# Performance work log

Measured on AMD Instinct MI355X. Metric: run time of the kernel, lower is better.

## Reference

```python
import jax, jax.numpy as jnp
import numpy as np

EPS = 1e-6


def setup_inputs() -> dict:
    key = jax.random.key(0)
    k1, k2, k3, k4 = jax.random.split(key, 4)
    B, N, D = 8, 4096, 512
    x = jax.random.normal(k1, (B, N, D), dtype=jnp.float32)
    # torch nn.Linear(dim, 3*dim, bias=False): weight shape [3D, D], y = x @ W.T
    w_qkv = jax.random.normal(k2, (3 * D, D), dtype=jnp.float32) * (1.0 / np.sqrt(D))
    w_proj = jax.random.normal(k3, (D, D), dtype=jnp.float32) * (1.0 / np.sqrt(D))
    b_proj = jax.random.normal(k4, (D,), dtype=jnp.float32) * 0.01
    return {"x": x, "w_qkv": w_qkv, "w_proj": w_proj, "b_proj": b_proj, "heads": 8}


def reference(x, w_qkv, w_proj, b_proj, heads):
    B, N, D = x.shape
    H = heads
    d = D // H
    # qkv projection -> (3, B, H, N, d)
    qkv = (x @ w_qkv.T).reshape(B, N, 3, H, d).transpose(2, 0, 3, 1, 4)
    q, k, v = qkv[0], qkv[1], qkv[2]
    # elu+1 feature map (positive features)
    q = jax.nn.elu(q) + 1.0 + EPS
    k = jax.nn.elu(k) + 1.0 + EPS
    # kv summary: [B,H,d,d]
    kv = jnp.einsum('bhnd,bhne->bhde', k, v)
    # denominator: q . sum_n(k) -> [B,H,N]
    denom = jnp.einsum('bhnd,bhd->bhn', q, k.sum(axis=2))
    out = jnp.einsum('bhnd,bhde->bhne', q, kv) / (denom[..., None] + EPS)
    out = out.transpose(0, 2, 1, 3).reshape(B, N, D)
    return out @ w_proj.T + b_proj
```

## Files before the change

kernel.cpp:

```cpp
#include <hip/hip_runtime.h>
#include <hip/hip_bf16.h>
#include <math.h>

#define EPSF 1e-6f

constexpr int Bc = 8;
constexpr int Nc = 4096;
constexpr int Dc = 512;
constexpr int QKVC = 3 * Dc;

typedef __attribute__((ext_vector_type(8))) short short8v;
typedef __attribute__((ext_vector_type(8))) unsigned short ushort8v;
typedef __attribute__((ext_vector_type(4))) float float4v;

__device__ __forceinline__ unsigned short f2bf(float f) {
    union { float f; unsigned int u; } v; v.f = f;
    unsigned int u = v.u;
    return (unsigned short)((u + 0x7fffu + ((u >> 16) & 1u)) >> 16);
}
__device__ __forceinline__ float bf2f(unsigned short h) {
    union { unsigned int u; float f; } v; v.u = ((unsigned int)h) << 16;
    return v.f;
}

typedef __attribute__((address_space(1))) const void gvoid_t;
typedef __attribute__((address_space(3))) void lvoid_t;
__device__ __forceinline__ void llds16(const void* g, void* l) {
    __builtin_amdgcn_global_load_lds((gvoid_t*)g, (lvoid_t*)l, 16, 0, 0);
}

__global__ __launch_bounds__(256) void cvt_f32_bf16(
    const float* __restrict__ in, unsigned short* __restrict__ out, int n8)
{
    int i = blockIdx.x * 256 + threadIdx.x;
    if (i >= n8) return;
    float4 a = reinterpret_cast<const float4*>(in)[2 * i];
    float4 b = reinterpret_cast<const float4*>(in)[2 * i + 1];
    ushort8v o;
    o[0] = f2bf(a.x); o[1] = f2bf(a.y); o[2] = f2bf(a.z); o[3] = f2bf(a.w);
    o[4] = f2bf(b.x); o[5] = f2bf(b.y); o[6] = f2bf(b.z); o[7] = f2bf(b.w);
    reinterpret_cast<ushort8v*>(out)[i] = o;
}

__global__ __launch_bounds__(256) void cvt_weights(
    const float* __restrict__ wq, const float* __restrict__ wp,
    unsigned short* __restrict__ wqo, unsigned short* __restrict__ wpo)
{
    const int i = blockIdx.x * 256 + threadIdx.x;
    const int NQ = 1536 * 512 / 8;
    const float* src; unsigned short* dst; int idx;
    if (i < NQ) { src = wq; dst = wqo; idx = i; }
    else        { src = wp; dst = wpo; idx = i - NQ; }
    float4 a = reinterpret_cast<const float4*>(src)[2 * idx];
    float4 b = reinterpret_cast<const float4*>(src)[2 * idx + 1];
    ushort8v o;
    o[0] = f2bf(a.x); o[1] = f2bf(a.y); o[2] = f2bf(a.z); o[3] = f2bf(a.w);
    o[4] = f2bf(b.x); o[5] = f2bf(b.y); o[6] = f2bf(b.z); o[7] = f2bf(b.w);
    reinterpret_cast<ushort8v*>(dst)[idx] = o;
}

__global__ __launch_bounds__(512, 2) void gemm_qkv(
    const unsigned short* __restrict__ A,
    const unsigned short* __restrict__ Bm,
    unsigned short* __restrict__ Cout)
{
    constexpr int LDA = 512, LDB = 512, LDC = 1536;
    constexpr int NT = 8;
    __shared__ unsigned short ring[3][24576];

    const int t = threadIdx.x;
    const int orig = blockIdx.x;
    const int wg = (orig & 7) * 192 + (orig >> 3);
    const int bm = (wg / 12) * 256;
    const int bn = (wg % 12) * 128;

    const int w = t >> 6, lane = t & 63;
    const int ln = lane & 15, g = lane >> 4;
    const int wr = (w >> 1) * 64;
    const int wc = (w & 1) * 64;
    const int l7 = ln & 7;

    const int rs = t >> 3;
    const int ci = t & 7;
    const int swz = ci ^ (rs & 7);
    const unsigned short* As0 = A + (size_t)(bm + rs) * LDA + swz * 8;
    const unsigned short* As1 = A + (size_t)(bm + 64 + rs) * LDA + swz * 8;
    const unsigned short* As2 = A + (size_t)(bm + 128 + rs) * LDA + swz * 8;
    const unsigned short* As3 = A + (size_t)(bm + 192 + rs) * LDA + swz * 8;
    const unsigned short* Bs0 = Bm + (size_t)(bn + rs) * LDB + swz * 8;
    const unsigned short* Bs1 = Bm + (size_t)(bn + 64 + rs) * LDB + swz * 8;

#define STAGEQ(Tt) do {                                                        \
        const int k0_ = (Tt) * 64;                                             \
        unsigned short* dA_ = &ring[(Tt) % 3][0];                              \
        unsigned short* dB_ = &ring[(Tt) % 3][16384];                          \
        llds16(As0 + k0_, dA_ + (size_t)t * 8);                                \
        llds16(As1 + k0_, dA_ + (size_t)(512 + t) * 8);                        \
        llds16(As2 + k0_, dA_ + (size_t)(1024 + t) * 8);                       \
        llds16(As3 + k0_, dA_ + (size_t)(1536 + t) * 8);                       \
        llds16(Bs0 + k0_, dB_ + (size_t)t * 8);                                \
        llds16(Bs1 + k0_, dB_ + (size_t)(512 + t) * 8);                        \
    } while (0)

    float4v acc[4][4];
#pragma unroll
    for (int i = 0; i < 4; ++i)
#pragma unroll
        for (int j = 0; j < 4; ++j) acc[i][j] = {0.f, 0.f, 0.f, 0.f};

    STAGEQ(0);
    STAGEQ(1);
    asm volatile("s_waitcnt vmcnt(6)" ::: "memory");
    __builtin_amdgcn_s_barrier();
    __builtin_amdgcn_sched_barrier(0);

#pragma unroll
    for (int T = 0; T < NT; ++T) {
        if (T + 2 < NT) STAGEQ(T + 2);

        const unsigned short* base = &ring[T % 3][0];
        short8v a[4][2], b[4][2];
#pragma unroll
        for (int i = 0; i < 4; ++i)
#pragma unroll
            for (int kk = 0; kk < 2; ++kk) {
                const int row = wr + i * 16 + ln;
                a[i][kk] = *reinterpret_cast<const short8v*>(
                    base + row * 64 + (((kk * 4 + g) ^ l7) << 3));
            }
#pragma unroll
        for (int j = 0; j < 4; ++j)
#pragma unroll
            for (int kk = 0; kk < 2; ++kk) {
                const int row = wc + j * 16 + ln;
                b[j][kk] = *reinterpret_cast<const short8v*>(
                    base + 16384 + row * 64 + (((kk * 4 + g) ^ l7) << 3));
            }

        __builtin_amdgcn_s_setprio(1);
#pragma unroll
        for (int kk = 0; kk < 2; ++kk)
#pragma unroll
            for (int i = 0; i < 4; ++i)
#pragma unroll
                for (int j = 0; j < 4; ++j)
                    acc[i][j] = __builtin_amdgcn_mfma_f32_16x16x32_bf16(
                        a[i][kk], b[j][kk], acc[i][j], 0, 0, 0);
        __builtin_amdgcn_s_setprio(0);

        if (T + 1 < NT) {
            if (T + 2 < NT)
                asm volatile("s_waitcnt vmcnt(6)" ::: "memory");
            else
                asm volatile("s_waitcnt vmcnt(0)" ::: "memory");
            __builtin_amdgcn_s_barrier();
            __builtin_amdgcn_sched_barrier(0);
        }
    }
#undef STAGEQ

#pragma unroll
    for (int i = 0; i < 4; ++i) {
        const int Rb = bm + wr + i * 16 + g * 4;
#pragma unroll
        for (int j = 0; j < 4; ++j) {
            const int Cc = bn + wc + j * 16 + ln;
            const bool do_elu = (Cc < 1024);
#pragma unroll
            for (int r = 0; r < 4; ++r) {
                float v = acc[i][j][r];
                if (do_elu) v = (v > 0.f) ? (v + 1.0f + EPSF) : (expf(v) + EPSF);
                Cout[(size_t)(Rb + r) * LDC + Cc] = f2bf(v);
            }
        }
    }
}

__global__ __launch_bounds__(256) void kv_part(
    const unsigned short* __restrict__ qkv,
    float* __restrict__ kvp, float* __restrict__ ksp)
{
    const int bh = blockIdx.x, chunk = blockIdx.y;
    const int b = bh >> 3, h = bh & 7;

    __shared__ float kt[64][68];
    __shared__ float vt[64][68];
    __shared__ float ksl[4][64];

    const int t  = threadIdx.x;
    const int e  = t & 63, dg = t >> 6;
    const int rr = t >> 3, slot = t & 7;

    float acc[16] = {};
    float ks = 0.f;

    const size_t base = ((size_t)b * Nc + (size_t)chunk * 512) * QKVC + h * 64;

    for (int n0 = 0; n0 < 512; n0 += 64) {
#pragma unroll
        for (int half = 0; half < 2; ++half) {
            const int row = rr + half * 32;
            const unsigned short* kr = qkv + base + (size_t)(n0 + row) * QKVC + Dc + slot * 8;
            const unsigned short* vr = kr + Dc;
            ushort8v kq = *reinterpret_cast<const ushort8v*>(kr);
            ushort8v vq = *reinterpret_cast<const ushort8v*>(vr);
            float4 k0 = make_float4(bf2f(kq[0]), bf2f(kq[1]), bf2f(kq[2]), bf2f(kq[3]));
            float4 k1 = make_float4(bf2f(kq[4]), bf2f(kq[5]), bf2f(kq[6]), bf2f(kq[7]));
            float4 v0 = make_float4(bf2f(vq[0]), bf2f(vq[1]), bf2f(vq[2]), bf2f(vq[3]));
            float4 v1 = make_float4(bf2f(vq[4]), bf2f(vq[5]), bf2f(vq[6]), bf2f(vq[7]));
            *reinterpret_cast<float4*>(&kt[row][slot * 8])     = k0;
            *reinterpret_cast<float4*>(&kt[row][slot * 8 + 4]) = k1;
            *reinterpret_cast<float4*>(&vt[row][slot * 8])     = v0;
            *reinterpret_cast<float4*>(&vt[row][slot * 8 + 4]) = v1;
        }
        __syncthreads();
#pragma unroll 2
        for (int nn = 0; nn < 64; ++nn) {
            const float vv = vt[nn][e];
            const float4 q0 = *reinterpret_cast<const float4*>(&kt[nn][dg * 16]);
            const float4 q1 = *reinterpret_cast<const float4*>(&kt[nn][dg * 16 + 4]);
            const float4 q2 = *reinterpret_cast<const float4*>(&kt[nn][dg * 16 + 8]);
            const float4 q3 = *reinterpret_cast<const float4*>(&kt[nn][dg * 16 + 12]);
            acc[0]  += q0.x * vv; acc[1]  += q0.y * vv; acc[2]  += q0.z * vv; acc[3]  += q0.w * vv;
            acc[4]  += q1.x * vv; acc[5]  += q1.y * vv; acc[6]  += q1.z * vv; acc[7]  += q1.w * vv;
            acc[8]  += q2.x * vv; acc[9]  += q2.y * vv; acc[10] += q2.z * vv; acc[11] += q2.w * vv;
            acc[12] += q3.x * vv; acc[13] += q3.y * vv; acc[14] += q3.z * vv; acc[15] += q3.w * vv;
        }
#pragma unroll
        for (int nn = 0; nn < 16; ++nn) ks += kt[dg * 16 + nn][e];
        __syncthreads();
    }

    float* kvpp = kvp + ((size_t)bh * 8 + chunk) * 4096;
#pragma unroll
    for (int i = 0; i < 16; ++i) kvpp[(dg * 16 + i) * 64 + e] = acc[i];

    ksl[dg][e] = ks;
    __syncthreads();
    if (t < 64) ksp[((size_t)bh * 8 + chunk) * 64 + t] =
        ksl[0][t] + ksl[1][t] + ksl[2][t] + ksl[3][t];
}

__global__ __launch_bounds__(256) void kv_reduce(
    const float* __restrict__ kvp, const float* __restrict__ ksp,
    unsigned short* __restrict__ kvb, float* __restrict__ ksum)
{
    const int bh = blockIdx.x, t = threadIdx.x;
    const float* src = kvp + (size_t)bh * 8 * 4096;
#pragma unroll
    for (int i = 0; i < 16; ++i) {
        const int idx = i * 256 + t;
        float s = 0.f;
#pragma unroll
        for (int c = 0; c < 8; ++c) s += src[c * 4096 + idx];
        kvb[(size_t)bh * 4096 + idx] = f2bf(s);
    }
    if (t < 64) {
        float s = 0.f;
#pragma unroll
        for (int c = 0; c < 8; ++c) s += ksp[((size_t)bh * 8 + c) * 64 + t];
        ksum[bh * 64 + t] = s;
    }
}

__global__ __launch_bounds__(256) void gemm_M(
    const unsigned short* __restrict__ kvb,
    const unsigned short* __restrict__ wp,
    unsigned short* __restrict__ MT)
{
    const int bh = blockIdx.x, b = bh >> 3, h = bh & 7;
    const int t = threadIdx.x, w = t >> 6, lane = t & 63;
    const int ln = lane & 15, g = lane >> 4;

    float4v acc[8][4];
#pragma unroll
    for (int i = 0; i < 8; ++i)
#pragma unroll
        for (int j = 0; j < 4; ++j) acc[i][j] = {0.f, 0.f, 0.f, 0.f};

#pragma unroll
    for (int kk = 0; kk < 2; ++kk) {
        short8v a[8], bf[4];
#pragma unroll
        for (int i = 0; i < 8; ++i)
            a[i] = *reinterpret_cast<const short8v*>(
                wp + (size_t)(w * 128 + i * 16 + ln) * 512 + h * 64 + kk * 32 + g * 8);
#pragma unroll
        for (int j = 0; j < 4; ++j)
            bf[j] = *reinterpret_cast<const short8v*>(
                kvb + (size_t)bh * 4096 + (j * 16 + ln) * 64 + kk * 32 + g * 8);
#pragma unroll
        for (int i = 0; i < 8; ++i)
#pragma unroll
            for (int j = 0; j < 4; ++j)
                acc[i][j] = __builtin_amdgcn_mfma_f32_16x16x32_bf16(a[i], bf[j], acc[i][j], 0, 0, 0);
    }

#pragma unroll
    for (int i = 0; i < 8; ++i) {
        const int c0 = w * 128 + i * 16 + g * 4;
#pragma unroll
        for (int j = 0; j < 4; ++j) {
            const int d = j * 16 + ln;
#pragma unroll
            for (int r = 0; r < 4; ++r)
                MT[(size_t)b * 262144 + (size_t)(c0 + r) * 512 + h * 64 + d] =
                    f2bf(acc[i][j][r]);
        }
    }
}

__global__ __launch_bounds__(256) void q_scale(
    unsigned short* __restrict__ qkv, const float* __restrict__ ksum)
{
    __shared__ float kss[512];
    const int blk = blockIdx.x;
    const int b = blk >> 7;
    const int t = threadIdx.x;
    kss[t] = ksum[b * 512 + t];
    kss[t + 256] = ksum[b * 512 + 256 + t];
    __syncthreads();

    const int row = blk * 32 + (t >> 3);
    const int h = t & 7;
    unsigned short* p = qkv + (size_t)row * QKVC + h * 64;

    ushort8v v[8];
#pragma unroll
    for (int s = 0; s < 8; ++s) v[s] = *reinterpret_cast<const ushort8v*>(p + s * 8);

    float den = EPSF;
#pragma unroll
    for (int s = 0; s < 8; ++s)
#pragma unroll
        for (int m = 0; m < 8; ++m)
            den += bf2f(v[s][m]) * kss[h * 64 + s * 8 + m];
    const float inv = 1.0f / den;

#pragma unroll
    for (int s = 0; s < 8; ++s) {
        ushort8v o;
#pragma unroll
        for (int m = 0; m < 8; ++m) o[m] = f2bf(bf2f(v[s][m]) * inv);
        *reinterpret_cast<ushort8v*>(p + s * 8) = o;
    }
}

__global__ __launch_bounds__(512, 2) void gemm_out(
    const unsigned short* __restrict__ A,
    const unsigned short* __restrict__ Bt,
    const float* __restrict__ bias,
    float* __restrict__ out)
{
    constexpr int LDA = 1536, LDB = 512, NT = 8;
    __shared__ unsigned short ring[3][24576];

    const int t = threadIdx.x;
    const int orig = blockIdx.x;
    const int wg = (orig & 7) * 64 + (orig >> 3);
    const int bm = (wg >> 2) * 256;
    const int bn = (wg & 3) * 128;
    const unsigned short* Bm = Bt + (size_t)(bm >> 12) * 262144;

    const int w = t >> 6, lane = t & 63;
    const int ln = lane & 15, g = lane >> 4;
    const int wr = (w >> 1) * 64;
    const int wc = (w & 1) * 64;
    const int l7 = ln & 7;

    const int rs = t >> 3;
    const int ci = t & 7;
    const int swz = ci ^ (rs & 7);
    const unsigned short* As0 = A + (size_t)(bm + rs) * LDA + swz * 8;
    const unsigned short* As1 = A + (size_t)(bm + 64 + rs) * LDA + swz * 8;
    const unsigned short* As2 = A + (size_t)(bm + 128 + rs) * LDA + swz * 8;
    const unsigned short* As3 = A + (size_t)(bm + 192 + rs) * LDA + swz * 8;
    const unsigned short* Bs0 = Bm + (size_t)(bn + rs) * LDB + swz * 8;
    const unsigned short* Bs1 = Bm + (size_t)(bn + 64 + rs) * LDB + swz * 8;

#define STAGEO(Tt) do {                                                        \
        const int k0_ = (Tt) * 64;                                             \
        unsigned short* dA_ = &ring[(Tt) % 3][0];                              \
        unsigned short* dB_ = &ring[(Tt) % 3][16384];                          \
        llds16(As0 + k0_, dA_ + (size_t)t * 8);                                \
        llds16(As1 + k0_, dA_ + (size_t)(512 + t) * 8);                        \
        llds16(As2 + k0_, dA_ + (size_t)(1024 + t) * 8);                       \
        llds16(As3 + k0_, dA_ + (size_t)(1536 + t) * 8);                       \
        llds16(Bs0 + k0_, dB_ + (size_t)t * 8);                                \
        llds16(Bs1 + k0_, dB_ + (size_t)(512 + t) * 8);                        \
    } while (0)

    float4v acc[4][4];
#pragma unroll
    for (int i = 0; i < 4; ++i)
#pragma unroll
        for (int j = 0; j < 4; ++j) acc[i][j] = {0.f, 0.f, 0.f, 0.f};

    STAGEO(0);
    STAGEO(1);
    asm volatile("s_waitcnt vmcnt(6)" ::: "memory");
    __builtin_amdgcn_s_barrier();
    __builtin_amdgcn_sched_barrier(0);

#pragma unroll
    for (int T = 0; T < NT; ++T) {
        if (T + 2 < NT) STAGEO(T + 2);

        const unsigned short* base = &ring[T % 3][0];
        short8v a[4][2], b[4][2];
#pragma unroll
        for (int i = 0; i < 4; ++i)
#pragma unroll
            for (int kk = 0; kk < 2; ++kk) {
                const int row = wr + i * 16 + ln;
                a[i][kk] = *reinterpret_cast<const short8v*>(
                    base + row * 64 + (((kk * 4 + g) ^ l7) << 3));
            }
#pragma unroll
        for (int j = 0; j < 4; ++j)
#pragma unroll
            for (int kk = 0; kk < 2; ++kk) {
                const int row = wc + j * 16 + ln;
                b[j][kk] = *reinterpret_cast<const short8v*>(
                    base + 16384 + row * 64 + (((kk * 4 + g) ^ l7) << 3));
            }

        __builtin_amdgcn_s_setprio(1);
#pragma unroll
        for (int kk = 0; kk < 2; ++kk)
#pragma unroll
            for (int i = 0; i < 4; ++i)
#pragma unroll
                for (int j = 0; j < 4; ++j)
                    acc[i][j] = __builtin_amdgcn_mfma_f32_16x16x32_bf16(
                        a[i][kk], b[j][kk], acc[i][j], 0, 0, 0);
        __builtin_amdgcn_s_setprio(0);

        if (T + 1 < NT) {
            if (T + 2 < NT)
                asm volatile("s_waitcnt vmcnt(6)" ::: "memory");
            else
                asm volatile("s_waitcnt vmcnt(0)" ::: "memory");
            __builtin_amdgcn_s_barrier();
            __builtin_amdgcn_sched_barrier(0);
        }
    }
#undef STAGEO

#pragma unroll
    for (int i = 0; i < 4; ++i) {
        const int Rb = bm + wr + i * 16 + g * 4;
#pragma unroll
        for (int j = 0; j < 4; ++j) {
            const int Cc = bn + wc + j * 16 + ln;
            const float bv = bias[Cc];
#pragma unroll
            for (int r = 0; r < 4; ++r)
                out[(size_t)(Rb + r) * 512 + Cc] = acc[i][j][r] + bv;
        }
    }
}

extern "C" void kernel_launch(void* const* d_in, const int* in_sizes, int n_in,
                              void* d_out, int out_size, void* d_ws, size_t ws_size,
                              hipStream_t stream)
{
    const float* x      = (const float*)d_in[0];
    const float* w_qkv  = (const float*)d_in[1];
    const float* w_proj = (const float*)d_in[2];
    const float* b_proj = (const float*)d_in[3];
    float* out = (float*)d_out;

    char* ws = (char*)d_ws;
    unsigned short* qkvb = (unsigned short*)ws;
    size_t off = (size_t)32768 * 1536 * 2;
    unsigned short* xb   = (unsigned short*)(ws + off); off += (size_t)32768 * 512 * 2;
    unsigned short* wqb  = (unsigned short*)(ws + off); off += (size_t)1536 * 512 * 2;
    unsigned short* wpb  = (unsigned short*)(ws + off); off += (size_t)512 * 512 * 2;
    float* kvp           = (float*)(ws + off);          off += (size_t)64 * 8 * 4096 * 4;
    float* ksp           = (float*)(ws + off);          off += (size_t)64 * 8 * 64 * 4;
    unsigned short* kvb  = (unsigned short*)(ws + off); off += (size_t)64 * 4096 * 2;
    float* ksumb         = (float*)(ws + off);          off += (size_t)64 * 64 * 4;
    unsigned short* MT   = (unsigned short*)(ws + off); off += (size_t)8 * 512 * 512 * 2;

    cvt_f32_bf16<<<dim3((32768 * 512 / 8 + 255) / 256), dim3(256), 0, stream>>>(x, xb, 32768 * 512 / 8);
    cvt_weights<<<dim3(((1536 * 512 + 512 * 512) / 8 + 255) / 256), dim3(256), 0, stream>>>(
        w_qkv, w_proj, wqb, wpb);

    gemm_qkv<<<dim3(1536), dim3(512), 0, stream>>>(xb, wqb, qkvb);

    kv_part<<<dim3(64, 8), dim3(256), 0, stream>>>(qkvb, kvp, ksp);
    kv_reduce<<<dim3(64), dim3(256), 0, stream>>>(kvp, ksp, kvb, ksumb);

    gemm_M<<<dim3(64), dim3(256), 0, stream>>>(kvb, wpb, MT);

    q_scale<<<dim3(1024), dim3(256), 0, stream>>>(qkvb, ksumb);

    gemm_out<<<dim3(512), dim3(512), 0, stream>>>(qkvb, MT, b_proj, out);
}
```

Measured before the change: 190.4 us.

## Fuse fp32-to-bf16 conversion of x into the QKV GEMM A-tile loading

Measured after the change: 197.2 us. 1.04x slower.

```diff
diff --git a/kernel.cpp b/kernel.cpp
--- a/kernel.cpp
+++ b/kernel.cpp
@@ -22,24 +22,16 @@
     union { unsigned int u; float f; } v; v.u = ((unsigned int)h) << 16;
     return v.f;
 }
+__device__ __forceinline__ unsigned int cvtpk(float lo, float hi) {
+    unsigned int r;
+    asm("v_cvt_pk_bf16_f32 %0, %1, %2" : "=v"(r) : "v"(lo), "v"(hi));
+    return r;
+}
 
 typedef __attribute__((address_space(1))) const void gvoid_t;
 typedef __attribute__((address_space(3))) void lvoid_t;
 __device__ __forceinline__ void llds16(const void* g, void* l) {
     __builtin_amdgcn_global_load_lds((gvoid_t*)g, (lvoid_t*)l, 16, 0, 0);
-}
-
-__global__ __launch_bounds__(256) void cvt_f32_bf16(
-    const float* __restrict__ in, unsigned short* __restrict__ out, int n8)
-{
-    int i = blockIdx.x * 256 + threadIdx.x;
-    if (i >= n8) return;
-    float4 a = reinterpret_cast<const float4*>(in)[2 * i];
-    float4 b = reinterpret_cast<const float4*>(in)[2 * i + 1];
-    ushort8v o;
-    o[0] = f2bf(a.x); o[1] = f2bf(a.y); o[2] = f2bf(a.z); o[3] = f2bf(a.w);
-    o[4] = f2bf(b.x); o[5] = f2bf(b.y); o[6] = f2bf(b.z); o[7] = f2bf(b.w);
-    reinterpret_cast<ushort8v*>(out)[i] = o;
 }
 
 __global__ __launch_bounds__(256) void cvt_weights(
@@ -60,7 +52,7 @@
 }
 
 __global__ __launch_bounds__(512, 2) void gemm_qkv(
-    const unsigned short* __restrict__ A,
+    const float* __restrict__ X,
     const unsigned short* __restrict__ Bm,
     unsigned short* __restrict__ Cout)
 {
@@ -83,40 +75,70 @@
     const int rs = t >> 3;
     const int ci = t & 7;
     const int swz = ci ^ (rs & 7);
-    const unsigned short* As0 = A + (size_t)(bm + rs) * LDA + swz * 8;
-    const unsigned short* As1 = A + (size_t)(bm + 64 + rs) * LDA + swz * 8;
-    const unsigned short* As2 = A + (size_t)(bm + 128 + rs) * LDA + swz * 8;
-    const unsigned short* As3 = A + (size_t)(bm + 192 + rs) * LDA + swz * 8;
+    const float* Xs0 = X + (size_t)(bm + rs) * LDA + swz * 8;
+    const float* Xs1 = X + (size_t)(bm + 64 + rs) * LDA + swz * 8;
+    const float* Xs2 = X + (size_t)(bm + 128 + rs) * LDA + swz * 8;
+    const float* Xs3 = X + (size_t)(bm + 192 + rs) * LDA + swz * 8;
     const unsigned short* Bs0 = Bm + (size_t)(bn + rs) * LDB + swz * 8;
     const unsigned short* Bs1 = Bm + (size_t)(bn + 64 + rs) * LDB + swz * 8;
 
-#define STAGEQ(Tt) do {                                                        \
+    float4 Ar[4][2];
+
+#define ISSUE_A(Tt) do {                                                       \
         const int k0_ = (Tt) * 64;                                             \
-        unsigned short* dA_ = &ring[(Tt) % 3][0];                              \
+        Ar[0][0] = *reinterpret_cast<const float4*>(Xs0 + k0_);                \
+        Ar[0][1] = *reinterpret_cast<const float4*>(Xs0 + k0_ + 4);            \
+        Ar[1][0] = *reinterpret_cast<const float4*>(Xs1 + k0_);                \
+        Ar[1][1] = *reinterpret_cast<const float4*>(Xs1 + k0_ + 4);            \
+        Ar[2][0] = *reinterpret_cast<const float4*>(Xs2 + k0_);                \
+        Ar[2][1] = *reinterpret_cast<const float4*>(Xs2 + k0_ + 4);            \
+        Ar[3][0] = *reinterpret_cast<const float4*>(Xs3 + k0_);                \
+        Ar[3][1] = *reinterpret_cast<const float4*>(Xs3 + k0_ + 4);            \
+    } while (0)
+
+#define STAGEB(Tt) do {                                                        \
+        const int k0_ = (Tt) * 64;                                             \
         unsigned short* dB_ = &ring[(Tt) % 3][16384];                          \
-        llds16(As0 + k0_, dA_ + (size_t)t * 8);                                \
-        llds16(As1 + k0_, dA_ + (size_t)(512 + t) * 8);                        \
-        llds16(As2 + k0_, dA_ + (size_t)(1024 + t) * 8);                       \
-        llds16(As3 + k0_, dA_ + (size_t)(1536 + t) * 8);                       \
         llds16(Bs0 + k0_, dB_ + (size_t)t * 8);                                \
         llds16(Bs1 + k0_, dB_ + (size_t)(512 + t) * 8);                        \
     } while (0)
 
+#define WRITE_A(Tt) do {                                                       \
+        unsigned short* dA_ = &ring[(Tt) % 3][0];                              \
+        uint4 w0, w1, w2, w3;                                                  \
+        w0.x = cvtpk(Ar[0][0].x, Ar[0][0].y); w0.y = cvtpk(Ar[0][0].z, Ar[0][0].w); \
+        w0.z = cvtpk(Ar[0][1].x, Ar[0][1].y); w0.w = cvtpk(Ar[0][1].z, Ar[0][1].w); \
+        w1.x = cvtpk(Ar[1][0].x, Ar[1][0].y); w1.y = cvtpk(Ar[1][0].z, Ar[1][0].w); \
+        w1.z = cvtpk(Ar[1][1].x, Ar[1][1].y); w1.w = cvtpk(Ar[1][1].z, Ar[1][1].w); \
+        w2.x = cvtpk(Ar[2][0].x, Ar[2][0].y); w2.y = cvtpk(Ar[2][0].z, Ar[2][0].w); \
+        w2.z = cvtpk(Ar[2][1].x, Ar[2][1].y); w2.w = cvtpk(Ar[2][1].z, Ar[2][1].w); \
+        w3.x = cvtpk(Ar[3][0].x, Ar[3][0].y); w3.y = cvtpk(Ar[3][0].z, Ar[3][0].w); \
+        w3.z = cvtpk(Ar[3][1].x, Ar[3][1].y); w3.w = cvtpk(Ar[3][1].z, Ar[3][1].w); \
+        *reinterpret_cast<uint4*>(dA_ + (size_t)t * 8)            = w0;        \
+        *reinterpret_cast<uint4*>(dA_ + (size_t)(512 + t) * 8)    = w1;        \
+        *reinterpret_cast<uint4*>(dA_ + (size_t)(1024 + t) * 8)   = w2;        \
+        *reinterpret_cast<uint4*>(dA_ + (size_t)(1536 + t) * 8)   = w3;        \
+    } while (0)
+
     float4v acc[4][4];
 #pragma unroll
     for (int i = 0; i < 4; ++i)
 #pragma unroll
         for (int j = 0; j < 4; ++j) acc[i][j] = {0.f, 0.f, 0.f, 0.f};
 
-    STAGEQ(0);
-    STAGEQ(1);
-    asm volatile("s_waitcnt vmcnt(6)" ::: "memory");
+    ISSUE_A(0);
+    STAGEB(0);
+    STAGEB(1);
+    asm volatile("s_waitcnt vmcnt(2)" ::: "memory");
+    WRITE_A(0);
+    asm volatile("s_waitcnt lgkmcnt(0)" ::: "memory");
     __builtin_amdgcn_s_barrier();
     __builtin_amdgcn_sched_barrier(0);
 
 #pragma unroll
     for (int T = 0; T < NT; ++T) {
-        if (T + 2 < NT) STAGEQ(T + 2);
+        if (T + 1 < NT) ISSUE_A(T + 1);
+        if (T + 2 < NT) STAGEB(T + 2);
 
         const unsigned short* base = &ring[T % 3][0];
         short8v a[4][2], b[4][2];
@@ -150,14 +172,18 @@
 
         if (T + 1 < NT) {
             if (T + 2 < NT)
-                asm volatile("s_waitcnt vmcnt(6)" ::: "memory");
+                asm volatile("s_waitcnt vmcnt(2)" ::: "memory");
             else
                 asm volatile("s_waitcnt vmcnt(0)" ::: "memory");
+            WRITE_A(T + 1);
+            asm volatile("s_waitcnt lgkmcnt(0)" ::: "memory");
             __builtin_amdgcn_s_barrier();
             __builtin_amdgcn_sched_barrier(0);
         }
     }
-#undef STAGEQ
+#undef ISSUE_A
+#undef STAGEB
+#undef WRITE_A
 
 #pragma unroll
     for (int i = 0; i < 4; ++i) {
@@ -474,7 +500,6 @@
     char* ws = (char*)d_ws;
     unsigned short* qkvb = (unsigned short*)ws;
     size_t off = (size_t)32768 * 1536 * 2;
-    unsigned short* xb   = (unsigned short*)(ws + off); off += (size_t)32768 * 512 * 2;
     unsigned short* wqb  = (unsigned short*)(ws + off); off += (size_t)1536 * 512 * 2;
     unsigned short* wpb  = (unsigned short*)(ws + off); off += (size_t)512 * 512 * 2;
     float* kvp           = (float*)(ws + off);          off += (size_t)64 * 8 * 4096 * 4;
@@ -483,11 +508,10 @@
     float* ksumb         = (float*)(ws + off);          off += (size_t)64 * 64 * 4;
     unsigned short* MT   = (unsigned short*)(ws + off); off += (size_t)8 * 512 * 512 * 2;
 
-    cvt_f32_bf16<<<dim3((32768 * 512 / 8 + 255) / 256), dim3(256), 0, stream>>>(x, xb, 32768 * 512 / 8);
     cvt_weights<<<dim3(((1536 * 512 + 512 * 512) / 8 + 255) / 256), dim3(256), 0, stream>>>(
         w_qkv, w_proj, wqb, wpb);
 
-    gemm_qkv<<<dim3(1536), dim3(512), 0, stream>>>(xb, wqb, qkvb);
+    gemm_qkv<<<dim3(1536), dim3(512), 0, stream>>>(x, wqb, qkvb);
 
     kv_part<<<dim3(64, 8), dim3(256), 0, stream>>>(qkvb, kvp, ksp);
     kv_reduce<<<dim3(64), dim3(256), 0, stream>>>(kvp, ksp, kvb, ksumb);
```
